# Optimization experiments

Hardware: AMD Instinct MI355X
Metric: run time of the kernel (lower is better)

The kernel has to match this reference:

```python
import jax, jax.numpy as jnp
import numpy as np

B, L, C = 8, 4096, 512
KS = (3, 5, 7)
EPS = 1e-5


def _layernorm(x, g, b):
    m = jnp.mean(x, axis=-1, keepdims=True)
    v = jnp.mean((x - m) ** 2, axis=-1, keepdims=True)
    return (x - m) / jnp.sqrt(v + EPS) * g + b


def _masked_conv(x1, ids, W, bias):
    # x1: [B, C, L], ids: [B, L] int32, W: [C, C, K], bias: [C]
    K = W.shape[-1]
    pl = (K - 1) // 2
    pr = (K - 1) - pl
    xp = jnp.pad(x1, ((0, 0), (0, 0), (pl, pr)))              # [B, C, L+K-1]
    ip = jnp.pad(ids, ((0, 0), (pl, pr)), constant_values=0)  # [B, L+K-1]
    Ldim = x1.shape[-1]
    # sliding windows via K static slices (unfold equivalent)
    Xw = jnp.stack([xp[:, :, k:k + Ldim] for k in range(K)], axis=-1)   # [B, C, L, K]
    Iw = jnp.stack([ip[:, k:k + Ldim] for k in range(K)], axis=-1)      # [B, L, K]
    center = K // 2
    mask = (Iw == Iw[:, :, center:center + 1]).astype(x1.dtype)         # [B, L, K]
    out = jnp.einsum('bcik,ock->boi', Xw * mask[:, None, :, :], W)
    return out + bias[None, :, None]


def setup_inputs() -> dict:
    key = jax.random.key(0)
    ks = jax.random.split(key, 16)
    x = jax.random.normal(ks[0], (B, L, C), dtype=jnp.float32)
    # contiguous chain segments per sample (equivalent to chain_idxs ranges)
    chain_idxs = jnp.sort(jax.random.randint(ks[1], (B, L), 0, 4), axis=1).astype(jnp.int32)
    inp = {'x': x, 'chain_idxs': chain_idxs}
    for i, K in enumerate(KS):
        inp[f'conv_w{i}'] = jax.random.normal(ks[2 + i], (C, C, K), dtype=jnp.float32)
        inp[f'conv_b{i}'] = jax.random.normal(ks[5 + i], (C,), dtype=jnp.float32)
    H = 4 * C
    lim_in = float(np.sqrt(6.0 / (C + H)))
    lim_out = float(np.sqrt(6.0 / (H + C)))
    inp['mlp_w_in'] = jax.random.uniform(ks[8], (C, H), jnp.float32, -lim_in, lim_in)
    inp['mlp_b_in'] = jnp.zeros((H,), jnp.float32)
    inp['mlp_w_out'] = jax.random.uniform(ks[9], (H, C), jnp.float32, -lim_out, lim_out)
    inp['mlp_b_out'] = jnp.zeros((C,), jnp.float32)
    inp['ln1_g'] = jnp.ones((C,), jnp.float32)
    inp['ln1_b'] = jnp.zeros((C,), jnp.float32)
    inp['ln2_g'] = jnp.ones((C,), jnp.float32)
    inp['ln2_b'] = jnp.zeros((C,), jnp.float32)
    return inp


def reference(x, chain_idxs, conv_w0, conv_b0, conv_w1, conv_b1, conv_w2, conv_b2,
              mlp_w_in, mlp_b_in, mlp_w_out, mlp_b_out, ln1_g, ln1_b, ln2_g, ln2_b):
    x1 = jnp.transpose(x, (0, 2, 1))  # [B, C, L]
    for W, bias in ((conv_w0, conv_b0), (conv_w1, conv_b1), (conv_w2, conv_b2)):
        x1 = _masked_conv(x1, chain_idxs, W, bias)
    h = _layernorm(x + jnp.transpose(x1, (0, 2, 1)), ln1_g, ln1_b)
    mlp = jax.nn.gelu(h @ mlp_w_in + mlp_b_in, approximate=False) @ mlp_w_out + mlp_b_out
    out = _layernorm(h + mlp, ln2_g, ln2_b)
    return out
```

## Files before the change

kernel.cpp:

```cpp
#include <hip/hip_runtime.h>
#include <hip/hip_bf16.h>
#include <math.h>

#define B_ 8
#define L_ 4096
#define C_ 512
#define H_ 2048
#define NPOS_ (B_*L_)

typedef __attribute__((ext_vector_type(8))) short short8;
typedef __attribute__((ext_vector_type(4))) float f32x4;

#define VMCNT(n) asm volatile("s_waitcnt vmcnt(" #n ")" ::: "memory")

__device__ __forceinline__ float bf2f(unsigned int u) {
    union { unsigned int u; float f; } c; c.u = u << 16; return c.f;
}
__device__ __forceinline__ unsigned short f2bf(float f) {
    union { float f; unsigned int u; } c; c.f = f;
    unsigned int r = c.u + 0x7fffu + ((c.u >> 16) & 1u);
    return (unsigned short)(r >> 16);
}

__device__ __forceinline__ void gload_lds16(const unsigned short* g, unsigned char* l) {
    __builtin_amdgcn_global_load_lds(
        (const __attribute__((address_space(1))) void*)g,
        (__attribute__((address_space(3))) void*)l, 16, 0, 0);
}


__global__ void __launch_bounds__(256) prep_conv_w(const float* __restrict__ W,
                                                   unsigned short* __restrict__ out, int K) {
    int idx = blockIdx.x * 256 + threadIdx.x;
    if (idx >= K * C_ * C_) return;
    int c = idx & (C_ - 1);
    int o = (idx >> 9) & (C_ - 1);
    int k = idx >> 18;
    out[idx] = f2bf(W[((size_t)o * C_ + c) * K + k]);
}

__global__ void __launch_bounds__(256) transpose_cast(const float* __restrict__ in,
                                                      unsigned short* __restrict__ out,
                                                      int R, int Cc) {
    __shared__ float tile[32][33];
    int tx = threadIdx.x & 31, ty = threadIdx.x >> 5;
    int c = blockIdx.x * 32 + tx;
    #pragma unroll
    for (int i = 0; i < 32; i += 8) {
        int r = blockIdx.y * 32 + ty + i;
        tile[ty + i][tx] = in[(size_t)r * Cc + c];
    }
    __syncthreads();
    #pragma unroll
    for (int i = 0; i < 32; i += 8) {
        int ro = blockIdx.x * 32 + ty + i;
        int co = blockIdx.y * 32 + tx;
        out[(size_t)ro * R + co] = f2bf(tile[tx][ty + i]);
    }
}

__global__ void __launch_bounds__(256) cast_f32_bf16(const float* __restrict__ in,
                                                     unsigned short* __restrict__ out, int n4) {
    int i = blockIdx.x * 256 + threadIdx.x;
    if (i >= n4) return;
    float4 v = ((const float4*)in)[i];
    uint2 o;
    o.x = (unsigned int)f2bf(v.x) | ((unsigned int)f2bf(v.y) << 16);
    o.y = (unsigned int)f2bf(v.z) | ((unsigned int)f2bf(v.w) << 16);
    ((uint2*)out)[i] = o;
}

template<int K>
__global__ void __launch_bounds__(256) conv_masked(const unsigned short* __restrict__ in,
                                                   const unsigned short* __restrict__ wt,
                                                   const float* __restrict__ bias,
                                                   const int* __restrict__ ids,
                                                   unsigned short* __restrict__ out) {
    constexpr int PL = (K - 1) / 2;
    constexpr int BM = 128, BN = 128;
    constexpr int ROWS = BM + K - 1;
    constexpr int ACH = (ROWS + 7) / 8;

    __shared__ __align__(16) unsigned char sA[ACH * 1024];
    __shared__ __align__(16) unsigned char sB[2][16 * 1024];
    __shared__ int sIds[ROWS];

    const int tid = threadIdx.x;
    const int wid = tid >> 6, lane = tid & 63;
    const int l15 = lane & 15, l4 = lane >> 4;
    const int r8 = lane >> 3, c8 = lane & 7;
    const int c16s = c8 ^ r8;
    const int i0 = blockIdx.x * BM;
    const int b = i0 >> 12;
    const int i0l = i0 & (L_ - 1);
    const int o0 = blockIdx.y * BN;
    const int wm = wid >> 1, wn = wid & 1;

    if (tid < ROWS) {
        int il = i0l + tid - PL;
        sIds[tid] = (il >= 0 && il < L_) ? ids[b * L_ + il] : -1;
    }
    __syncthreads();

    unsigned int mbits[4];
    #pragma unroll
    for (int mf = 0; mf < 4; ++mf) {
        int p = wm * 64 + mf * 16 + l15;
        int ctr = sIds[p + PL];
        unsigned int m = 0;
        #pragma unroll
        for (int k = 0; k < K; ++k)
            if (sIds[p + k] == ctr) m |= (1u << k);
        mbits[mf] = m;
    }

    f32x4 acc[4][4];
    #pragma unroll
    for (int i = 0; i < 4; ++i)
        #pragma unroll
        for (int j = 0; j < 4; ++j) acc[i][j] = 0.f;

    const short8 zero8 = 0;

    for (int cc = 0; cc < 8; ++cc) {
        #pragma unroll
        for (int it = 0; it < 5; ++it) {
            int chunk = wid + it * 4;
            if (chunk < ACH) {
                int row = chunk * 8 + r8;
                int il = i0l + row - PL;
                il = il < 0 ? 0 : (il >= L_ ? L_ - 1 : il);
                gload_lds16(in + ((size_t)(b * L_ + il) * C_ + cc * 64 + c16s * 8),
                            sA + chunk * 1024);
            }
        }
        const unsigned short* wcc = wt + (size_t)o0 * C_ + cc * 64;
        #pragma unroll
        for (int it = 0; it < 4; ++it) {
            int chunk = wid * 4 + it;
            int row = chunk * 8 + r8;
            gload_lds16(wcc + (size_t)row * C_ + c16s * 8, sB[0] + chunk * 1024);
        }

        #pragma unroll
        for (int k = 0; k < K; ++k) {
            if (k + 1 < K) {
                const unsigned short* wkb = wcc + (size_t)(k + 1) * C_ * C_;
                #pragma unroll
                for (int it = 0; it < 4; ++it) {
                    int chunk = wid * 4 + it;
                    int row = chunk * 8 + r8;
                    gload_lds16(wkb + (size_t)row * C_ + c16s * 8,
                                sB[(k + 1) & 1] + chunk * 1024);
                }
                VMCNT(4);
            } else {
                VMCNT(0);
            }
            __builtin_amdgcn_s_barrier();
            const unsigned char* bbuf = sB[k & 1];
            #pragma unroll
            for (int kk = 0; kk < 2; ++kk) {
                short8 af[4];
                #pragma unroll
                for (int mf = 0; mf < 4; ++mf) {
                    int row = wm * 64 + mf * 16 + l15 + k;
                    int addr = (row * 128 + kk * 64 + l4 * 16) ^ ((row & 7) << 4);
                    short8 a = *(const short8*)(sA + addr);
                    af[mf] = ((mbits[mf] >> k) & 1u) ? a : zero8;
                }
                #pragma unroll
                for (int nf = 0; nf < 4; ++nf) {
                    int col = wn * 64 + nf * 16 + l15;
                    int addr = (col * 128 + kk * 64 + l4 * 16) ^ ((col & 7) << 4);
                    short8 bfr = *(const short8*)(bbuf + addr);
                    #pragma unroll
                    for (int mf = 0; mf < 4; ++mf)
                        acc[mf][nf] = __builtin_amdgcn_mfma_f32_16x16x32_bf16(af[mf], bfr, acc[mf][nf], 0, 0, 0);
                }
            }
            __builtin_amdgcn_s_barrier();
        }
    }

    #pragma unroll
    for (int mf = 0; mf < 4; ++mf)
        #pragma unroll
        for (int nf = 0; nf < 4; ++nf) {
            int col = o0 + wn * 64 + nf * 16 + l15;
            float bv = bias[col];
            #pragma unroll
            for (int j = 0; j < 4; ++j) {
                int p = i0 + wm * 64 + mf * 16 + l4 * 4 + j;
                out[(size_t)p * C_ + col] = f2bf(acc[mf][nf][j] + bv);
            }
        }
}


__global__ void __launch_bounds__(256) ln1_kernel(const float* __restrict__ x,
                                                  const unsigned short* __restrict__ cv,
                                                  const float* __restrict__ g,
                                                  const float* __restrict__ bb,
                                                  unsigned short* __restrict__ hb) {
    __shared__ float red[8];
    int row = blockIdx.x, t = threadIdx.x;
    size_t base = (size_t)row * C_;
    float2 xv = *(const float2*)(x + base + t * 2);
    unsigned int cu = *(const unsigned int*)(cv + base + t * 2);
    float s0 = xv.x + bf2f(cu & 0xffffu);
    float s1 = xv.y + bf2f(cu >> 16);
    float ss = s0 + s1;
    #pragma unroll
    for (int off = 32; off; off >>= 1) ss += __shfl_down(ss, off);
    if ((t & 63) == 0) red[t >> 6] = ss;
    __syncthreads();
    if (t == 0) red[4] = (red[0] + red[1] + red[2] + red[3]) * (1.f / C_);
    __syncthreads();
    float mean = red[4];
    float d0 = s0 - mean, d1 = s1 - mean;
    float vv = d0 * d0 + d1 * d1;
    #pragma unroll
    for (int off = 32; off; off >>= 1) vv += __shfl_down(vv, off);
    if ((t & 63) == 0) red[t >> 6] = vv;
    __syncthreads();
    if (t == 0) red[5] = (red[0] + red[1] + red[2] + red[3]) * (1.f / C_);
    __syncthreads();
    float rstd = rsqrtf(red[5] + 1e-5f);
    float2 gv = *(const float2*)(g + t * 2);
    float2 bv = *(const float2*)(bb + t * 2);
    float h0 = d0 * rstd * gv.x + bv.x;
    float h1 = d1 * rstd * gv.y + bv.y;
    *(unsigned int*)(hb + base + t * 2) =
        (unsigned int)f2bf(h0) | ((unsigned int)f2bf(h1) << 16);
}

__global__ void __launch_bounds__(256) ln2_bf16(const unsigned short* __restrict__ yb,
                                                const float* __restrict__ g,
                                                const float* __restrict__ bb,
                                                float* __restrict__ outp) {
    __shared__ float red[8];
    int row = blockIdx.x, t = threadIdx.x;
    size_t base = (size_t)row * C_;
    unsigned int yu = *(const unsigned int*)(yb + base + t * 2);
    float y0 = bf2f(yu & 0xffffu), y1 = bf2f(yu >> 16);
    float ss = y0 + y1;
    #pragma unroll
    for (int off = 32; off; off >>= 1) ss += __shfl_down(ss, off);
    if ((t & 63) == 0) red[t >> 6] = ss;
    __syncthreads();
    if (t == 0) red[4] = (red[0] + red[1] + red[2] + red[3]) * (1.f / C_);
    __syncthreads();
    float mean = red[4];
    float d0 = y0 - mean, d1 = y1 - mean;
    float vv = d0 * d0 + d1 * d1;
    #pragma unroll
    for (int off = 32; off; off >>= 1) vv += __shfl_down(vv, off);
    if ((t & 63) == 0) red[t >> 6] = vv;
    __syncthreads();
    if (t == 0) red[5] = (red[0] + red[1] + red[2] + red[3]) * (1.f / C_);
    __syncthreads();
    float rstd = rsqrtf(red[5] + 1e-5f);
    float2 gv = *(const float2*)(g + t * 2);
    float2 bv = *(const float2*)(bb + t * 2);
    float2 o;
    o.x = d0 * rstd * gv.x + bv.x;
    o.y = d1 * rstd * gv.y + bv.y;
    *(float2*)(outp + base + t * 2) = o;
}

template<int MODE, int BM, int BN>
__global__ void __launch_bounds__(256) gemm_bf16(const unsigned short* __restrict__ A,
                                                 const unsigned short* __restrict__ BT,
                                                 const float* __restrict__ bias,
                                                 unsigned short* __restrict__ res_io,
                                                 unsigned short* __restrict__ outp,
                                                 int Nd, int Kd) {
    constexpr int MI = BM / 32, NI = BN / 32;
    __shared__ __align__(16) unsigned char sA[2][BM * 128];
    __shared__ __align__(16) unsigned char sBT[2][BN * 128];
    const int tid = threadIdx.x;
    const int wid = tid >> 6, lane = tid & 63;
    const int l15 = lane & 15, l4 = lane >> 4;
    const int r8 = lane >> 3, c8 = lane & 7;
    const int c16s = c8 ^ r8;
    const int m0 = blockIdx.x * BM, n0 = blockIdx.y * BN;
    const int wm = wid >> 1, wn = wid & 1;

    f32x4 acc[MI][NI];
    #pragma unroll
    for (int i = 0; i < MI; ++i)
        #pragma unroll
        for (int j = 0; j < NI; ++j) acc[i][j] = 0.f;

    const int nk = Kd / 64;
    auto stage = [&](int kc, int bi) {
        const unsigned short* Ab = A + (size_t)m0 * Kd + kc * 64;
        const unsigned short* Bb = BT + (size_t)n0 * Kd + kc * 64;
        #pragma unroll
        for (int it = 0; it < MI; ++it) {
            int chunk = wid * MI + it;
            int row = chunk * 8 + r8;
            gload_lds16(Ab + (size_t)row * Kd + c16s * 8, sA[bi] + chunk * 1024);
        }
        #pragma unroll
        for (int it = 0; it < NI; ++it) {
            int chunk = wid * NI + it;
            int row = chunk * 8 + r8;
            gload_lds16(Bb + (size_t)row * Kd + c16s * 8, sBT[bi] + chunk * 1024);
        }
    };

    stage(0, 0);
    for (int kc = 0; kc < nk; ++kc) {
        if (kc + 1 < nk) {
            stage(kc + 1, (kc + 1) & 1);
            if constexpr (MI + NI == 8) VMCNT(8); else VMCNT(6);
        } else {
            VMCNT(0);
        }
        __builtin_amdgcn_s_barrier();
        const unsigned char* a_ = sA[kc & 1];
        const unsigned char* b_ = sBT[kc & 1];
        #pragma unroll
        for (int kk = 0; kk < 2; ++kk) {
            short8 af[MI], bf[NI];
            #pragma unroll
            for (int i = 0; i < MI; ++i) {
                int row = wm * (BM / 2) + i * 16 + l15;
                af[i] = *(const short8*)(a_ + ((row * 128 + kk * 64 + l4 * 16) ^ ((row & 7) << 4)));
            }
            #pragma unroll
            for (int j = 0; j < NI; ++j) {
                int col = wn * (BN / 2) + j * 16 + l15;
                bf[j] = *(const short8*)(b_ + ((col * 128 + kk * 64 + l4 * 16) ^ ((col & 7) << 4)));
            }
            #pragma unroll
            for (int i = 0; i < MI; ++i)
                #pragma unroll
                for (int j = 0; j < NI; ++j)
                    acc[i][j] = __builtin_amdgcn_mfma_f32_16x16x32_bf16(af[i], bf[j], acc[i][j], 0, 0, 0);
        }
        __builtin_amdgcn_s_barrier();
    }

    #pragma unroll
    for (int i = 0; i < MI; ++i)
        #pragma unroll
        for (int j = 0; j < NI; ++j) {
            int col = n0 + wn * (BN / 2) + j * 16 + l15;
            float bv = bias[col];
            #pragma unroll
            for (int jj = 0; jj < 4; ++jj) {
                int row = m0 + wm * (BM / 2) + i * 16 + l4 * 4 + jj;
                size_t idx = (size_t)row * Nd + col;
                float v = acc[i][j][jj] + bv;
                if (MODE == 0) {
                    v = 0.5f * v * (1.0f + erff(v * 0.70710678118654752f));
                    outp[idx] = f2bf(v);
                } else {
                    v += bf2f((unsigned int)res_io[idx]);
                    res_io[idx] = f2bf(v);
                }
            }
        }
}


extern "C" void kernel_launch(void* const* d_in, const int* in_sizes, int n_in,
                              void* d_out, int out_size, void* d_ws, size_t ws_size,
                              hipStream_t stream) {
    (void)in_sizes; (void)n_in; (void)out_size; (void)ws_size;
    const float* x    = (const float*)d_in[0];
    const int*   ids  = (const int*)d_in[1];
    const float* cw0  = (const float*)d_in[2];
    const float* cb0  = (const float*)d_in[3];
    const float* cw1  = (const float*)d_in[4];
    const float* cb1  = (const float*)d_in[5];
    const float* cw2  = (const float*)d_in[6];
    const float* cb2  = (const float*)d_in[7];
    const float* w_in = (const float*)d_in[8];
    const float* b_in = (const float*)d_in[9];
    const float* w_out= (const float*)d_in[10];
    const float* b_out= (const float*)d_in[11];
    const float* ln1g = (const float*)d_in[12];
    const float* ln1b = (const float*)d_in[13];
    const float* ln2g = (const float*)d_in[14];
    const float* ln2b = (const float*)d_in[15];

    char* ws = (char*)d_ws;
    size_t off = 0;
    auto alloc = [&](size_t bytes) { void* p = ws + off; off += (bytes + 255) & ~(size_t)255; return p; };
    unsigned short* wconv = (unsigned short*)alloc((size_t)15 * C_ * C_ * 2);
    unsigned short* wint  = (unsigned short*)alloc((size_t)H_ * C_ * 2);
    unsigned short* woutt = (unsigned short*)alloc((size_t)C_ * H_ * 2);
    unsigned short* hb    = (unsigned short*)alloc((size_t)NPOS_ * C_ * 2);
    constexpr int MCH = NPOS_ / 4;
    unsigned short* hid   = (unsigned short*)alloc((size_t)MCH * H_ * 2);

    unsigned short* act0 = (unsigned short*)d_out;
    unsigned short* act1 = act0 + (size_t)NPOS_ * C_;

    prep_conv_w<<<(3 * C_ * C_ + 255) / 256, 256, 0, stream>>>(cw0, wconv, 3);
    prep_conv_w<<<(5 * C_ * C_ + 255) / 256, 256, 0, stream>>>(cw1, wconv + (size_t)3 * C_ * C_, 5);
    prep_conv_w<<<(7 * C_ * C_ + 255) / 256, 256, 0, stream>>>(cw2, wconv + (size_t)8 * C_ * C_, 7);
    transpose_cast<<<dim3(H_ / 32, C_ / 32), 256, 0, stream>>>(w_in, wint, C_, H_);
    transpose_cast<<<dim3(C_ / 32, H_ / 32), 256, 0, stream>>>(w_out, woutt, H_, C_);
    cast_f32_bf16<<<(NPOS_ * C_ / 4 + 255) / 256, 256, 0, stream>>>(x, act0, NPOS_ * C_ / 4);

    conv_masked<3><<<dim3(NPOS_ / 128, C_ / 128), 256, 0, stream>>>(act0, wconv, cb0, ids, act1);
    conv_masked<5><<<dim3(NPOS_ / 128, C_ / 128), 256, 0, stream>>>(act1, wconv + (size_t)3 * C_ * C_, cb1, ids, act0);
    conv_masked<7><<<dim3(NPOS_ / 128, C_ / 128), 256, 0, stream>>>(act0, wconv + (size_t)8 * C_ * C_, cb2, ids, act1);

    ln1_kernel<<<NPOS_, 256, 0, stream>>>(x, act1, ln1g, ln1b, hb);

    for (int ch = 0; ch < 4; ++ch) {
        unsigned short* hbc = hb + (size_t)ch * MCH * C_;
        gemm_bf16<0, 128, 128><<<dim3(MCH / 128, H_ / 128), 256, 0, stream>>>(
            hbc, wint, b_in, nullptr, hid, H_, C_);
        gemm_bf16<1, 64, 128><<<dim3(MCH / 64, C_ / 128), 256, 0, stream>>>(
            hid, woutt, b_out, hbc, nullptr, C_, H_);
    }

    ln2_bf16<<<NPOS_, 256, 0, stream>>>(hb, ln2g, ln2b, (float*)d_out);
}
```

Measured before the change: 618.8 us.

## Add unmasked conv fast path, tanh-style GELU, and larger MLP chunks in output buffer

The masked conv now takes a wave-uniform branch that skips per-fragment mask selects when every row in the wave has a full window mask. The exact erf GELU is replaced by a sigmoid-form tanh approximation built on __expf. The MLP hidden buffer moves into the output buffer, which allows 2 chunks instead of 4 and so fewer, larger GEMM launches. The GELU approximation differs from the exact erf reference, and the conv fast path adds code size and register pressure.

```diff
diff --git a/kernel.cpp b/kernel.cpp
--- a/kernel.cpp
+++ b/kernel.cpp
@@ -96,9 +96,9 @@
     const int o0 = blockIdx.y * BN;
     const int wm = wid >> 1, wn = wid & 1;
 
-    if (tid < ROWS) {
-        int il = i0l + tid - PL;
-        sIds[tid] = (il >= 0 && il < L_) ? ids[b * L_ + il] : -1;
+    for (int r = tid; r < ROWS; r += 256) {
+        int il = i0l + r - PL;
+        sIds[r] = (il >= 0 && il < L_) ? ids[b * L_ + il] : -1;
     }
     __syncthreads();
 
@@ -113,6 +113,8 @@
             if (sIds[p + k] == ctr) m |= (1u << k);
         mbits[mf] = m;
     }
+    constexpr unsigned int FULLM = (1u << K) - 1u;
+    const bool fastmask = __all((mbits[0] & mbits[1] & mbits[2] & mbits[3]) == FULLM);
 
     f32x4 acc[4][4];
     #pragma unroll
@@ -159,24 +161,46 @@
             }
             __builtin_amdgcn_s_barrier();
             const unsigned char* bbuf = sB[k & 1];
-            #pragma unroll
-            for (int kk = 0; kk < 2; ++kk) {
-                short8 af[4];
+            if (fastmask) {
                 #pragma unroll
-                for (int mf = 0; mf < 4; ++mf) {
-                    int row = wm * 64 + mf * 16 + l15 + k;
-                    int addr = (row * 128 + kk * 64 + l4 * 16) ^ ((row & 7) << 4);
-                    short8 a = *(const short8*)(sA + addr);
-                    af[mf] = ((mbits[mf] >> k) & 1u) ? a : zero8;
+                for (int kk = 0; kk < 2; ++kk) {
+                    short8 af[4];
+                    #pragma unroll
+                    for (int mf = 0; mf < 4; ++mf) {
+                        int row = wm * 64 + mf * 16 + l15 + k;
+                        int addr = (row * 128 + kk * 64 + l4 * 16) ^ ((row & 7) << 4);
+                        af[mf] = *(const short8*)(sA + addr);
+                    }
+                    #pragma unroll
+                    for (int nf = 0; nf < 4; ++nf) {
+                        int col = wn * 64 + nf * 16 + l15;
+                        int addr = (col * 128 + kk * 64 + l4 * 16) ^ ((col & 7) << 4);
+                        short8 bfr = *(const short8*)(bbuf + addr);
+                        #pragma unroll
+                        for (int mf = 0; mf < 4; ++mf)
+                            acc[mf][nf] = __builtin_amdgcn_mfma_f32_16x16x32_bf16(af[mf], bfr, acc[mf][nf], 0, 0, 0);
+                    }
                 }
+            } else {
                 #pragma unroll
-                for (int nf = 0; nf < 4; ++nf) {
-                    int col = wn * 64 + nf * 16 + l15;
-                    int addr = (col * 128 + kk * 64 + l4 * 16) ^ ((col & 7) << 4);
-                    short8 bfr = *(const short8*)(bbuf + addr);
+                for (int kk = 0; kk < 2; ++kk) {
+                    short8 af[4];
                     #pragma unroll
-                    for (int mf = 0; mf < 4; ++mf)
-                        acc[mf][nf] = __builtin_amdgcn_mfma_f32_16x16x32_bf16(af[mf], bfr, acc[mf][nf], 0, 0, 0);
+                    for (int mf = 0; mf < 4; ++mf) {
+                        int row = wm * 64 + mf * 16 + l15 + k;
+                        int addr = (row * 128 + kk * 64 + l4 * 16) ^ ((row & 7) << 4);
+                        short8 a = *(const short8*)(sA + addr);
+                        af[mf] = ((mbits[mf] >> k) & 1u) ? a : zero8;
+                    }
+                    #pragma unroll
+                    for (int nf = 0; nf < 4; ++nf) {
+                        int col = wn * 64 + nf * 16 + l15;
+                        int addr = (col * 128 + kk * 64 + l4 * 16) ^ ((col & 7) << 4);
+                        short8 bfr = *(const short8*)(bbuf + addr);
+                        #pragma unroll
+                        for (int mf = 0; mf < 4; ++mf)
+                            acc[mf][nf] = __builtin_amdgcn_mfma_f32_16x16x32_bf16(af[mf], bfr, acc[mf][nf], 0, 0, 0);
+                    }
                 }
             }
             __builtin_amdgcn_s_barrier();
@@ -356,7 +380,9 @@
                 size_t idx = (size_t)row * Nd + col;
                 float v = acc[i][j][jj] + bv;
                 if (MODE == 0) {
-                    v = 0.5f * v * (1.0f + erff(v * 0.70710678118654752f));
+                    float e = __expf(v * (1.5957691216057308f
+                                          + 0.07135481627f * v * v));
+                    v = v * e / (e + 1.0f);
                     outp[idx] = f2bf(v);
                 } else {
                     v += bf2f((unsigned int)res_io[idx]);
@@ -395,11 +421,11 @@
     unsigned short* wint  = (unsigned short*)alloc((size_t)H_ * C_ * 2);
     unsigned short* woutt = (unsigned short*)alloc((size_t)C_ * H_ * 2);
     unsigned short* hb    = (unsigned short*)alloc((size_t)NPOS_ * C_ * 2);
-    constexpr int MCH = NPOS_ / 4;
-    unsigned short* hid   = (unsigned short*)alloc((size_t)MCH * H_ * 2);
 
     unsigned short* act0 = (unsigned short*)d_out;
     unsigned short* act1 = act0 + (size_t)NPOS_ * C_;
+    unsigned short* hid  = (unsigned short*)d_out;
+    constexpr int MCH = NPOS_ / 2;
 
     prep_conv_w<<<(3 * C_ * C_ + 255) / 256, 256, 0, stream>>>(cw0, wconv, 3);
     prep_conv_w<<<(5 * C_ * C_ + 255) / 256, 256, 0, stream>>>(cw1, wconv + (size_t)3 * C_ * C_, 5);
@@ -414,7 +440,7 @@
 
     ln1_kernel<<<NPOS_, 256, 0, stream>>>(x, act1, ln1g, ln1b, hb);
 
-    for (int ch = 0; ch < 4; ++ch) {
+    for (int ch = 0; ch < 2; ++ch) {
         unsigned short* hbc = hb + (size_t)ch * MCH * C_;
         gemm_bf16<0, 128, 128><<<dim3(MCH / 128, H_ / 128), 256, 0, stream>>>(
             hbc, wint, b_in, nullptr, hid, H_, C_);
```

Measured after the change: 770.1 us. 24.5% more time.
